# Optimization experiments

Hardware: AMD Instinct MI355X
Metric: run time of the kernel (lower is better)

Reference implementation:

```python
import jax, jax.numpy as jnp
import numpy as np

NUM_EMBEDDINGS = 512
EMBEDDING_DIM = 64
COMMITMENT_COST = 0.25
DECAY = 0.99
EPSILON = 1e-05


def setup_inputs() -> dict:
    key = jax.random.key(0)
    k1, k2, k3 = jax.random.split(key, 3)
    inputs = jax.random.normal(k1, (32, 64, 64, EMBEDDING_DIM), dtype=jnp.float32)
    emb_w = jax.random.normal(k2, (NUM_EMBEDDINGS, EMBEDDING_DIM), dtype=jnp.float32)
    ema_cluster_size = jnp.ones((NUM_EMBEDDINGS,), dtype=jnp.float32)
    ema_w = jax.random.normal(k3, (NUM_EMBEDDINGS, EMBEDDING_DIM), dtype=jnp.float32)
    return {"inputs": inputs, "emb_w": emb_w,
            "ema_cluster_size": ema_cluster_size, "ema_w": ema_w}


def reference(inputs, emb_w, ema_cluster_size, ema_w):
    """VQ-VAE EMA quantizer forward (training=True path).

    inputs:           [B, H, W, D]  NHWC latents
    emb_w:            [K, D]        codebook (pre-update)
    ema_cluster_size: [K]           EMA cluster-size buffer
    ema_w:            [K, D]        EMA weight buffer
    """
    B, H, W, D = inputs.shape
    K = emb_w.shape[0]
    flat = inputs.reshape(-1, D)                                  # [N, D]

    distances = (jnp.sum(flat * flat, axis=1, keepdims=True)
                 - 2.0 * flat @ emb_w.T
                 + jnp.sum(emb_w * emb_w, axis=1))
    encoding_indices = jnp.argmin(distances, axis=1)              # [N]
    encodings = jax.nn.one_hot(encoding_indices, K, dtype=flat.dtype)  # [N, K]

    # --- EMA codebook update (buffer math; no gradient flows here) ---
    counts = jax.lax.stop_gradient(jnp.sum(encodings, axis=0))    # [K]
    cs = ema_cluster_size * DECAY + (1.0 - DECAY) * counts
    n = jnp.sum(cs)
    cs = (cs + EPSILON) / (n + K * EPSILON) * n                   # Laplace smoothing
    dw = jax.ops.segment_sum(jax.lax.stop_gradient(flat),
                             encoding_indices, num_segments=K)    # [K, D]
    new_ema_w = ema_w * DECAY + (1.0 - DECAY) * dw
    new_emb = new_ema_w / cs[:, None]                             # updated codebook

    # Quantize with the updated codebook (gather)
    quantized = new_emb[encoding_indices].reshape(B, H, W, D)

    # Commitment loss (quantized is detached)
    e_latent_loss = jnp.mean((jax.lax.stop_gradient(quantized) - inputs) ** 2)
    loss = COMMITMENT_COST * e_latent_loss

    # Straight-through estimator
    quantized_st = inputs + jax.lax.stop_gradient(quantized - inputs)

    avg_probs = jnp.mean(encodings, axis=0)
    perplexity = jnp.exp(-jnp.sum(avg_probs * jnp.log(avg_probs + 1e-10)))

    # NHWC -> NCHW as in the original return
    return loss, jnp.transpose(quantized_st, (0, 3, 1, 2)), perplexity, encodings
```

## Files before the change

### kernel.cpp

```cpp
#include <hip/hip_runtime.h>

#define DIM 64
#define K_CODES 512
#define N_VEC 131072
#define NREP 16
#define Q_OFF 1
#define PERP_OFF 8388609
#define ENC_OFF 8388610

using bfrag = __attribute__((ext_vector_type(8))) short;
using ffrag = __attribute__((ext_vector_type(4))) float;

__device__ __forceinline__ void split3(float x, short& h0, short& h1, short& h2)
{
    unsigned u0 = __float_as_uint(x);
    h0 = (short)(u0 >> 16);
    float r = x - __uint_as_float(u0 & 0xFFFF0000u);
    unsigned u1 = __float_as_uint(r);
    h1 = (short)(u1 >> 16);
    float r2 = r - __uint_as_float(u1 & 0xFFFF0000u);
    h2 = (short)(__float_as_uint(r2) >> 16);
}

__global__ __launch_bounds__(256) void enc_zero_kernel(float* __restrict__ enc)
{
    const size_t nf4 = 16777215;
    float4* body = reinterpret_cast<float4*>(enc + 2);
    const size_t stride = (size_t)gridDim.x * 256;
    const float4 z = make_float4(0.f, 0.f, 0.f, 0.f);
    for (size_t i = (size_t)blockIdx.x * 256 + threadIdx.x; i < nf4; i += stride)
        body[i] = z;
    if (blockIdx.x == 0 && threadIdx.x == 0) {
        enc[0] = 0.f; enc[1] = 0.f;
        enc[67108862] = 0.f; enc[67108863] = 0.f;
    }
}

__global__ __launch_bounds__(64) void ee_kernel(const float* __restrict__ emb_w,
                                                float* __restrict__ ee)
{
    const int k = blockIdx.x * 64 + threadIdx.x;
    const float4* e4 = reinterpret_cast<const float4*>(emb_w + (size_t)k * DIM);
    float s0 = 0, s1 = 0, s2 = 0, s3 = 0;
#pragma unroll
    for (int d4 = 0; d4 < 16; ++d4) {
        const float4 v = e4[d4];
        s0 = fmaf(v.x, v.x, s0); s1 = fmaf(v.y, v.y, s1);
        s2 = fmaf(v.z, v.z, s2); s3 = fmaf(v.w, v.w, s3);
    }
    ee[k] = (s0 + s1) + (s2 + s3);
}

__global__ __launch_bounds__(256) void epack_kernel(const float* __restrict__ emb_w,
                                                    bfrag* __restrict__ epack)
{
    const int t = blockIdx.x * 256 + threadIdx.x;
    const int lane = t & 63;
    const int db = (t >> 6) & 1;
    const int ct = t >> 7;
    const int c  = ct * 16 + (lane & 15);
    const int d0 = db * 32 + (lane >> 4) * 8;
    const float* src = emb_w + (size_t)c * DIM + d0;
    bfrag f0, f1, f2;
#pragma unroll
    for (int j = 0; j < 8; ++j) {
        short a, b, cc;
        split3(src[j], a, b, cc);
        f0[j] = a; f1[j] = b; f2[j] = cc;
    }
    const int base = (ct * 2 + db) * 3;
    epack[(base + 0) * 64 + lane] = f0;
    epack[(base + 1) * 64 + lane] = f1;
    epack[(base + 2) * 64 + lane] = f2;
}

__global__ __launch_bounds__(256, 1) void argmin_mfma_kernel(
    const float* __restrict__ inputs,
    const bfrag* __restrict__ epack,
    const float* __restrict__ eeg,
    int* __restrict__ idx,
    float* __restrict__ counts_rep,
    float* __restrict__ enc)
{
    const int t = threadIdx.x;
    const int w = t >> 6;
    const int lane = t & 63;
    const int r16 = lane & 15;
    const int quad = lane >> 4;
    const size_t v0 = (size_t)blockIdx.x * 128 + w * 32;

    bfrag xf[2][2][3];
#pragma unroll
    for (int rt = 0; rt < 2; ++rt)
#pragma unroll
        for (int db = 0; db < 2; ++db) {
            const float* src = inputs + (v0 + rt * 16 + r16) * DIM + db * 32 + quad * 8;
            const float4 va = *reinterpret_cast<const float4*>(src);
            const float4 vb = *reinterpret_cast<const float4*>(src + 4);
            float vals[8] = {va.x, va.y, va.z, va.w, vb.x, vb.y, vb.z, vb.w};
            bfrag f0, f1, f2;
#pragma unroll
            for (int j = 0; j < 8; ++j) {
                short a, b, c;
                split3(vals[j], a, b, c);
                f0[j] = a; f1[j] = b; f2[j] = c;
            }
            xf[rt][db][0] = f0; xf[rt][db][1] = f1; xf[rt][db][2] = f2;
        }

    float best[2][4];
    int bestk[2][4];
#pragma unroll
    for (int a = 0; a < 2; ++a)
#pragma unroll
        for (int b = 0; b < 4; ++b) { best[a][b] = 3.4e38f; bestk[a][b] = 0; }

    constexpr int PI[6] = {0, 0, 1, 0, 2, 1};
    constexpr int PJ[6] = {0, 1, 0, 2, 0, 1};

    bfrag eC[2][3];
    float eelC;
#pragma unroll
    for (int db = 0; db < 2; ++db)
#pragma unroll
        for (int s = 0; s < 3; ++s)
            eC[db][s] = epack[(db * 3 + s) * 64 + lane];
    eelC = eeg[r16];

    for (int ct = 0; ct < 32; ++ct) {
        bfrag eN[2][3];
        float eelN = 0.f;
        if (ct < 31) {
#pragma unroll
            for (int db = 0; db < 2; ++db)
#pragma unroll
                for (int s = 0; s < 3; ++s)
                    eN[db][s] = epack[(((ct + 1) * 2 + db) * 3 + s) * 64 + lane];
            eelN = eeg[(ct + 1) * 16 + r16];
        }

        ffrag acc[2];
        acc[0] = (ffrag){0.f, 0.f, 0.f, 0.f};
        acc[1] = (ffrag){0.f, 0.f, 0.f, 0.f};
#pragma unroll
        for (int db = 0; db < 2; ++db)
#pragma unroll
            for (int p = 0; p < 6; ++p) {
                acc[0] = __builtin_amdgcn_mfma_f32_16x16x32_bf16(
                    xf[0][db][PI[p]], eC[db][PJ[p]], acc[0], 0, 0, 0);
                acc[1] = __builtin_amdgcn_mfma_f32_16x16x32_bf16(
                    xf[1][db][PI[p]], eC[db][PJ[p]], acc[1], 0, 0, 0);
            }

        const int kc = ct * 16 + r16;
#pragma unroll
        for (int rt = 0; rt < 2; ++rt)
#pragma unroll
            for (int rg = 0; rg < 4; ++rg) {
                const float dist = fmaf(-2.f, acc[rt][rg], eelC);
                if (dist < best[rt][rg]) { best[rt][rg] = dist; bestk[rt][rg] = kc; }
            }

#pragma unroll
        for (int db = 0; db < 2; ++db)
#pragma unroll
            for (int s = 0; s < 3; ++s)
                eC[db][s] = eN[db][s];
        eelC = eelN;
    }

#pragma unroll
    for (int rt = 0; rt < 2; ++rt)
#pragma unroll
        for (int rg = 0; rg < 4; ++rg) {
            float b = best[rt][rg];
            int k = bestk[rt][rg];
#pragma unroll
            for (int m = 1; m < 16; m <<= 1) {
                const float ob = __shfl_xor(b, m, 64);
                const int ok = __shfl_xor(k, m, 64);
                if (ob < b || (ob == b && ok < k)) { b = ob; k = ok; }
            }
            bestk[rt][rg] = k;
        }

    if (r16 == 0) {
        float* crep = counts_rep + (blockIdx.x & (NREP - 1)) * K_CODES;
#pragma unroll
        for (int rt = 0; rt < 2; ++rt)
#pragma unroll
            for (int rg = 0; rg < 4; ++rg) {
                const int v = rt * 16 + quad * 4 + rg;
                const int k = bestk[rt][rg];
                idx[v0 + v] = k;
                atomicAdd(&crep[k], 1.0f);
                enc[(v0 + v) * (size_t)K_CODES + k] = 1.0f;
            }
    }
}

__global__ __launch_bounds__(256) void dw_scatter_kernel(
    const float* __restrict__ inputs,
    const int* __restrict__ idx,
    float* __restrict__ dwrep)
{
    __shared__ int sIdx[256];
    const int t = threadIdx.x;
    const size_t vbase = (size_t)blockIdx.x * 256;
    sIdx[t] = idx[vbase + t];
    __syncthreads();
    const int w = t >> 6, lane = t & 63;
    const int v0 = w * 64;
#pragma unroll 4
    for (int j = 0; j < 64; ++j) {
        const int v = v0 + j;
        const int k = sIdx[v];
        const float xv = inputs[(vbase + v) * DIM + lane];
        atomicAdd(&dwrep[((v & (NREP - 1)) << 15) + (k << 6) + lane], xv);
    }
}

__global__ __launch_bounds__(512) void emaA_kernel(
    const float* __restrict__ counts_rep,
    const float* __restrict__ ema_cs,
    float* __restrict__ csbuf,
    float* __restrict__ perp_out)
{
    __shared__ float red[K_CODES];
    const int k = threadIdx.x;
    float cnt = 0.f;
#pragma unroll
    for (int r = 0; r < NREP; ++r) cnt += counts_rep[r * K_CODES + k];
    float cs = ema_cs[k] * 0.99f + 0.01f * cnt;

    red[k] = cs;
    __syncthreads();
    for (int s = K_CODES / 2; s > 0; s >>= 1) {
        if (k < s) red[k] += red[k + s];
        __syncthreads();
    }
    const float n = red[0];
    __syncthreads();

    csbuf[k] = (cs + 1e-5f) / (n + (float)K_CODES * 1e-5f) * n;

    const float p = cnt * (1.0f / (float)N_VEC);
    red[k] = p * logf(p + 1e-10f);
    __syncthreads();
    for (int s = K_CODES / 2; s > 0; s >>= 1) {
        if (k < s) red[k] += red[k + s];
        __syncthreads();
    }
    if (k == 0) perp_out[0] = expf(-red[0]);
}

__global__ __launch_bounds__(256) void emaB_kernel(
    const float* __restrict__ dwrep,
    const float* __restrict__ ema_w,
    const float* __restrict__ csbuf,
    float* __restrict__ new_emb)
{
    const int t = blockIdx.x * 256 + threadIdx.x;
    const int k = t >> 6;
    float dwv = 0.f;
#pragma unroll
    for (int r = 0; r < NREP; ++r) dwv += dwrep[(r << 15) + t];
    const float v = ema_w[t] * 0.99f + 0.01f * dwv;
    new_emb[t] = v / csbuf[k];
}

__global__ __launch_bounds__(256) void quantize_kernel(
    const float* __restrict__ inputs,
    const int* __restrict__ idx,
    const float* __restrict__ new_emb,
    float* __restrict__ out_q,
    float* __restrict__ loss_accum)
{
    __shared__ int sIdx[64];
    __shared__ float tile[DIM][65];
    __shared__ float wsum[4];

    const int bh = blockIdx.x;
    const int b = bh >> 6, h = bh & 63;
    const int t = threadIdx.x;

    if (t < 64) sIdx[t] = idx[bh * 64 + t];
    __syncthreads();

    const float* inRow = inputs + (size_t)bh * 64 * DIM;
    const int d = t & 63;
    const int wg = t >> 6;
    float lsum = 0.f;
#pragma unroll
    for (int p = 0; p < 16; ++p) {
        const int w = wg * 16 + p;
        const float xv = inRow[w * DIM + d];
        const float qv = new_emb[sIdx[w] * DIM + d];
        const float diff = qv - xv;
        tile[d][w] = xv + diff;
        lsum = fmaf(diff, diff, lsum);
    }
    __syncthreads();

    const int w2 = t & 63;
    const int dg = t >> 6;
#pragma unroll
    for (int p = 0; p < 16; ++p) {
        const int d2 = dg * 16 + p;
        out_q[(((size_t)b * DIM + d2) * 64 + h) * 64 + w2] = tile[d2][w2];
    }

    for (int off = 32; off > 0; off >>= 1) lsum += __shfl_down(lsum, off);
    if ((t & 63) == 0) wsum[t >> 6] = lsum;
    __syncthreads();
    if (t == 0) atomicAdd(loss_accum, (wsum[0] + wsum[1]) + (wsum[2] + wsum[3]));
}

__global__ void finalize_kernel(const float* __restrict__ loss_accum,
                                float* __restrict__ out_loss)
{
    out_loss[0] = 0.25f * (loss_accum[0] / 8388608.0f);
}

extern "C" void kernel_launch(void* const* d_in, const int* in_sizes, int n_in,
                              void* d_out, int out_size, void* d_ws, size_t ws_size,
                              hipStream_t stream)
{
    const float* inputs = (const float*)d_in[0];
    const float* emb_w  = (const float*)d_in[1];
    const float* ema_cs = (const float*)d_in[2];
    const float* ema_w  = (const float*)d_in[3];
    float* out = (float*)d_out;
    float* ws  = (float*)d_ws;

    int*   idxbuf  = (int*)ws;
    float* crep    = ws + 131072;
    float* lossac  = ws + 139264;
    float* csbuf   = ws + 139265;
    float* eebuf   = ws + 139777;
    float* nemb    = ws + 140289;
    bfrag* epack   = (bfrag*)(ws + 173060);

    float* dwrep = out + 16;

    hipMemsetAsync(crep, 0, (NREP * K_CODES + 1) * sizeof(float), stream);
    hipMemsetAsync(dwrep, 0, NREP * K_CODES * DIM * sizeof(float), stream);

    ee_kernel<<<K_CODES / 64, 64, 0, stream>>>(emb_w, eebuf);
    epack_kernel<<<16, 256, 0, stream>>>(emb_w, epack);

    enc_zero_kernel<<<2048, 256, 0, stream>>>(out + ENC_OFF);

    argmin_mfma_kernel<<<N_VEC / 128, 256, 0, stream>>>(
        inputs, epack, eebuf, idxbuf, crep, out + ENC_OFF);

    dw_scatter_kernel<<<N_VEC / 256, 256, 0, stream>>>(inputs, idxbuf, dwrep);

    emaA_kernel<<<1, K_CODES, 0, stream>>>(crep, ema_cs, csbuf, out + PERP_OFF);
    emaB_kernel<<<K_CODES * DIM / 256, 256, 0, stream>>>(dwrep, ema_w, csbuf, nemb);

    quantize_kernel<<<32 * 64, 256, 0, stream>>>(
        inputs, idxbuf, nemb, out + Q_OFF, lossac);

    finalize_kernel<<<1, 1, 0, stream>>>(lossac, out);
}
```

Measured before the change: 226.0 us.

## Fuse codebook prep kernels, widen dw replicas, raise argmin occupancy

Merges the codebook norm and bf16 split-pack kernels into one launch, and zeroes the dw replica buffer inside the encoding-zero kernel instead of a separate memset. Increases dw scatter replicas from 16 to 64 to reduce atomic contention. Drops the manual register double-buffering in the argmin loop and sets launch bounds to allow 4 blocks per CU, trading prefetch for occupancy. The larger replica buffer adds more zeroing and reduction traffic.

```diff
diff --git a/kernel.cpp b/kernel.cpp
--- a/kernel.cpp
+++ b/kernel.cpp
@@ -3,7 +3,8 @@
 #define DIM 64
 #define K_CODES 512
 #define N_VEC 131072
-#define NREP 16
+#define CREP 16
+#define DREP 64
 #define Q_OFF 1
 #define PERP_OFF 8388609
 #define ENC_OFF 8388610
@@ -22,7 +23,51 @@
     h2 = (short)(__float_as_uint(r2) >> 16);
 }
 
-__global__ __launch_bounds__(256) void enc_zero_kernel(float* __restrict__ enc)
+__global__ __launch_bounds__(256) void epack_ee_kernel(
+    const float* __restrict__ emb_w,
+    bfrag* __restrict__ epack,
+    float* __restrict__ ee)
+{
+    __shared__ float part[2][16][8];
+    const int tl = threadIdx.x;
+    const int t = blockIdx.x * 256 + tl;
+    const int lane = t & 63;
+    const int db = (t >> 6) & 1;
+    const int ctl = tl >> 7;
+    const int ct = t >> 7;
+    const int r16 = lane & 15, quad = lane >> 4;
+    const int c  = ct * 16 + r16;
+    const int d0 = db * 32 + quad * 8;
+    const float* src = emb_w + (size_t)c * DIM + d0;
+
+    bfrag f0, f1, f2;
+    float ssum = 0.f;
+#pragma unroll
+    for (int j = 0; j < 8; ++j) {
+        const float x = src[j];
+        ssum = fmaf(x, x, ssum);
+        short a, b, cc;
+        split3(x, a, b, cc);
+        f0[j] = a; f1[j] = b; f2[j] = cc;
+    }
+    const int base = (ct * 2 + db) * 3;
+    epack[(base + 0) * 64 + lane] = f0;
+    epack[(base + 1) * 64 + lane] = f1;
+    epack[(base + 2) * 64 + lane] = f2;
+
+    part[ctl][r16][db * 4 + quad] = ssum;
+    __syncthreads();
+    if (tl < 32) {
+        const int cl = tl >> 4, r = tl & 15;
+        float s = 0.f;
+#pragma unroll
+        for (int i = 0; i < 8; ++i) s += part[cl][r][i];
+        ee[(blockIdx.x * 2 + cl) * 16 + r] = s;
+    }
+}
+
+__global__ __launch_bounds__(256) void enc_zero_kernel(float* __restrict__ enc,
+                                                       float* __restrict__ dwrep)
 {
     const size_t nf4 = 16777215;
     float4* body = reinterpret_cast<float4*>(enc + 2);
@@ -30,51 +75,17 @@
     const float4 z = make_float4(0.f, 0.f, 0.f, 0.f);
     for (size_t i = (size_t)blockIdx.x * 256 + threadIdx.x; i < nf4; i += stride)
         body[i] = z;
+    float4* dw4 = reinterpret_cast<float4*>(dwrep);
+    const size_t ndw4 = (size_t)DREP * K_CODES * DIM / 4;
+    for (size_t i = (size_t)blockIdx.x * 256 + threadIdx.x; i < ndw4; i += stride)
+        dw4[i] = z;
     if (blockIdx.x == 0 && threadIdx.x == 0) {
         enc[0] = 0.f; enc[1] = 0.f;
         enc[67108862] = 0.f; enc[67108863] = 0.f;
     }
 }
 
-__global__ __launch_bounds__(64) void ee_kernel(const float* __restrict__ emb_w,
-                                                float* __restrict__ ee)
-{
-    const int k = blockIdx.x * 64 + threadIdx.x;
-    const float4* e4 = reinterpret_cast<const float4*>(emb_w + (size_t)k * DIM);
-    float s0 = 0, s1 = 0, s2 = 0, s3 = 0;
-#pragma unroll
-    for (int d4 = 0; d4 < 16; ++d4) {
-        const float4 v = e4[d4];
-        s0 = fmaf(v.x, v.x, s0); s1 = fmaf(v.y, v.y, s1);
-        s2 = fmaf(v.z, v.z, s2); s3 = fmaf(v.w, v.w, s3);
-    }
-    ee[k] = (s0 + s1) + (s2 + s3);
-}
-
-__global__ __launch_bounds__(256) void epack_kernel(const float* __restrict__ emb_w,
-                                                    bfrag* __restrict__ epack)
-{
-    const int t = blockIdx.x * 256 + threadIdx.x;
-    const int lane = t & 63;
-    const int db = (t >> 6) & 1;
-    const int ct = t >> 7;
-    const int c  = ct * 16 + (lane & 15);
-    const int d0 = db * 32 + (lane >> 4) * 8;
-    const float* src = emb_w + (size_t)c * DIM + d0;
-    bfrag f0, f1, f2;
-#pragma unroll
-    for (int j = 0; j < 8; ++j) {
-        short a, b, cc;
-        split3(src[j], a, b, cc);
-        f0[j] = a; f1[j] = b; f2[j] = cc;
-    }
-    const int base = (ct * 2 + db) * 3;
-    epack[(base + 0) * 64 + lane] = f0;
-    epack[(base + 1) * 64 + lane] = f1;
-    epack[(base + 2) * 64 + lane] = f2;
-}
-
-__global__ __launch_bounds__(256, 1) void argmin_mfma_kernel(
+__global__ __launch_bounds__(256, 4) void argmin_mfma_kernel(
     const float* __restrict__ inputs,
     const bfrag* __restrict__ epack,
     const float* __restrict__ eeg,
@@ -83,11 +94,11 @@
     float* __restrict__ enc)
 {
     const int t = threadIdx.x;
-    const int w = t >> 6;
+    const int wv = t >> 6;
     const int lane = t & 63;
     const int r16 = lane & 15;
     const int quad = lane >> 4;
-    const size_t v0 = (size_t)blockIdx.x * 128 + w * 32;
+    const size_t v0 = (size_t)blockIdx.x * 128 + wv * 32;
 
     bfrag xf[2][2][3];
 #pragma unroll
@@ -118,26 +129,14 @@
     constexpr int PI[6] = {0, 0, 1, 0, 2, 1};
     constexpr int PJ[6] = {0, 1, 0, 2, 0, 1};
 
-    bfrag eC[2][3];
-    float eelC;
-#pragma unroll
-    for (int db = 0; db < 2; ++db)
-#pragma unroll
-        for (int s = 0; s < 3; ++s)
-            eC[db][s] = epack[(db * 3 + s) * 64 + lane];
-    eelC = eeg[r16];
-
     for (int ct = 0; ct < 32; ++ct) {
-        bfrag eN[2][3];
-        float eelN = 0.f;
-        if (ct < 31) {
-#pragma unroll
-            for (int db = 0; db < 2; ++db)
-#pragma unroll
-                for (int s = 0; s < 3; ++s)
-                    eN[db][s] = epack[(((ct + 1) * 2 + db) * 3 + s) * 64 + lane];
-            eelN = eeg[(ct + 1) * 16 + r16];
-        }
+        bfrag e[2][3];
+#pragma unroll
+        for (int db = 0; db < 2; ++db)
+#pragma unroll
+            for (int s = 0; s < 3; ++s)
+                e[db][s] = epack[((ct * 2 + db) * 3 + s) * 64 + lane];
+        const float eel = eeg[ct * 16 + r16];
 
         ffrag acc[2];
         acc[0] = (ffrag){0.f, 0.f, 0.f, 0.f};
@@ -147,9 +146,9 @@
 #pragma unroll
             for (int p = 0; p < 6; ++p) {
                 acc[0] = __builtin_amdgcn_mfma_f32_16x16x32_bf16(
-                    xf[0][db][PI[p]], eC[db][PJ[p]], acc[0], 0, 0, 0);
+                    xf[0][db][PI[p]], e[db][PJ[p]], acc[0], 0, 0, 0);
                 acc[1] = __builtin_amdgcn_mfma_f32_16x16x32_bf16(
-                    xf[1][db][PI[p]], eC[db][PJ[p]], acc[1], 0, 0, 0);
+                    xf[1][db][PI[p]], e[db][PJ[p]], acc[1], 0, 0, 0);
             }
 
         const int kc = ct * 16 + r16;
@@ -157,16 +156,9 @@
         for (int rt = 0; rt < 2; ++rt)
 #pragma unroll
             for (int rg = 0; rg < 4; ++rg) {
-                const float dist = fmaf(-2.f, acc[rt][rg], eelC);
+                const float dist = fmaf(-2.f, acc[rt][rg], eel);
                 if (dist < best[rt][rg]) { best[rt][rg] = dist; bestk[rt][rg] = kc; }
             }
-
-#pragma unroll
-        for (int db = 0; db < 2; ++db)
-#pragma unroll
-            for (int s = 0; s < 3; ++s)
-                eC[db][s] = eN[db][s];
-        eelC = eelN;
     }
 
 #pragma unroll
@@ -185,7 +177,7 @@
         }
 
     if (r16 == 0) {
-        float* crep = counts_rep + (blockIdx.x & (NREP - 1)) * K_CODES;
+        float* crep = counts_rep + (blockIdx.x & (CREP - 1)) * K_CODES;
 #pragma unroll
         for (int rt = 0; rt < 2; ++rt)
 #pragma unroll
@@ -216,7 +208,7 @@
         const int v = v0 + j;
         const int k = sIdx[v];
         const float xv = inputs[(vbase + v) * DIM + lane];
-        atomicAdd(&dwrep[((v & (NREP - 1)) << 15) + (k << 6) + lane], xv);
+        atomicAdd(&dwrep[((size_t)(v & (DREP - 1)) << 15) + (k << 6) + lane], xv);
     }
 }
 
@@ -230,7 +222,7 @@
     const int k = threadIdx.x;
     float cnt = 0.f;
 #pragma unroll
-    for (int r = 0; r < NREP; ++r) cnt += counts_rep[r * K_CODES + k];
+    for (int r = 0; r < CREP; ++r) cnt += counts_rep[r * K_CODES + k];
     float cs = ema_cs[k] * 0.99f + 0.01f * cnt;
 
     red[k] = cs;
@@ -264,7 +256,7 @@
     const int k = t >> 6;
     float dwv = 0.f;
 #pragma unroll
-    for (int r = 0; r < NREP; ++r) dwv += dwrep[(r << 15) + t];
+    for (int r = 0; r < DREP; ++r) dwv += dwrep[((size_t)r << 15) + t];
     const float v = ema_w[t] * 0.99f + 0.01f * dwv;
     new_emb[t] = v / csbuf[k];
 }
@@ -343,13 +335,11 @@
 
     float* dwrep = out + 16;
 
-    hipMemsetAsync(crep, 0, (NREP * K_CODES + 1) * sizeof(float), stream);
-    hipMemsetAsync(dwrep, 0, NREP * K_CODES * DIM * sizeof(float), stream);
-
-    ee_kernel<<<K_CODES / 64, 64, 0, stream>>>(emb_w, eebuf);
-    epack_kernel<<<16, 256, 0, stream>>>(emb_w, epack);
-
-    enc_zero_kernel<<<2048, 256, 0, stream>>>(out + ENC_OFF);
+    hipMemsetAsync(crep, 0, (CREP * K_CODES + 1) * sizeof(float), stream);
+
+    epack_ee_kernel<<<16, 256, 0, stream>>>(emb_w, epack, eebuf);
+
+    enc_zero_kernel<<<2048, 256, 0, stream>>>(out + ENC_OFF, dwrep);
 
     argmin_mfma_kernel<<<N_VEC / 128, 256, 0, stream>>>(
         inputs, epack, eebuf, idxbuf, crep, out + ENC_OFF);
```

Measured after the change: 235.0 us. +4.0%, slower.
